# Performance work log

Measured on AMD Instinct MI355X. Metric: run time of the kernel, lower is better.

## Reference

```python
import jax, jax.numpy as jnp
import numpy as np


def _nearest_resize(x, Hl, Wl):
    # x: [B, Hf, Wf] -> [B, Hl, Wl], PyTorch F.interpolate(mode='nearest') semantics:
    # src_idx = floor(out_idx * in_size / out_size)
    B, Hf, Wf = x.shape
    ri = (jnp.arange(Hl) * Hf) // Hl
    ci = (jnp.arange(Wl) * Wf) // Wl
    return x[:, ri[:, None], ci[None, :]]


def _nearest_centroid(f, c):
    # f: [B, C, H, W], c: [K, C]
    # argmin_k ||f - c_k||_2 over channels == argmin of squared distance
    f2 = jnp.sum(f * f, axis=1)                       # [B, H, W]
    c2 = jnp.sum(c * c, axis=1)                       # [K]
    cross = jnp.einsum('bchw,kc->bkhw', f, c)         # [B, K, H, W]
    d2 = f2[:, None] - 2.0 * cross + c2[None, :, None, None]
    return jnp.argmin(d2, axis=1)                     # [B, H, W] int


def setup_inputs() -> dict:
    key = jax.random.key(0)
    k1, k2, k3, k4, k5, k6 = jax.random.split(key, 6)
    B, C, Hf, Wf = 4, 256, 64, 128
    K = 19  # class_num
    Hl, Wl = 512, 1024
    return {
        'feature_s2t': jax.random.normal(k1, (B, C, Hf, Wf), dtype=jnp.float32),
        'feature_target': jax.random.normal(k2, (B, C, Hf, Wf), dtype=jnp.float32),
        'label_s2t': jax.random.randint(k3, (B, Hl, Wl), 0, K, dtype=jnp.int64) if jax.config.jax_enable_x64 else jax.random.randint(k3, (B, Hl, Wl), 0, K, dtype=jnp.int32),
        'label_target': jax.random.randint(k4, (B, Hl, Wl), 0, K, dtype=jnp.int32),
        'centroid_s2t': jax.random.normal(k5, (K, C), dtype=jnp.float32),
        'centroid_target': jax.random.normal(k6, (K, C), dtype=jnp.float32),
    }


def reference(feature_s2t, feature_target, label_s2t, label_target, centroid_s2t, centroid_target):
    # feature_s2t is matched against the TARGET-domain centroids and vice versa
    # (cross assignment, exactly as in the torch forward).
    mask_s2t = _nearest_centroid(feature_s2t, centroid_target)     # [B, Hf, Wf]
    mask_target = _nearest_centroid(feature_target, centroid_s2t)  # [B, Hf, Wf]
    Hl, Wl = label_s2t.shape[1], label_s2t.shape[2]
    mask_s2t = _nearest_resize(mask_s2t, Hl, Wl).astype(jnp.int32)
    Hl2, Wl2 = label_target.shape[1], label_target.shape[2]
    mask_target = _nearest_resize(mask_target, Hl2, Wl2).astype(jnp.int32)
    return (mask_s2t, mask_target)
```

## Files before the change

kernel.cpp:

```cpp
#include <hip/hip_runtime.h>

#define K   19
#define C   256
#define HF  64
#define WF  128
#define HW  (HF * WF)
#define BB  4
#define HL  512
#define WL  1024

#define TAU 0.03f

#define CPAD 264
#define DPAD 66

typedef __attribute__((ext_vector_type(8)))  short bf16x8;
typedef __attribute__((ext_vector_type(16))) float f32x16;

__global__ __launch_bounds__(256, 4) void centroid_mask_kernel(
    const float* __restrict__ feat0,
    const float* __restrict__ feat1,
    const float* __restrict__ cent0,
    const float* __restrict__ cent1,
    int* __restrict__ out)
{
    __shared__ __align__(16) unsigned short chi[K * CPAD];
    __shared__ __align__(16) unsigned short clo[K * CPAD];
    __shared__ float  dbuf[4][16][DPAD];
    __shared__ double c2p[K][8];
    __shared__ double sc2d[K];
    __shared__ float  sc2f[K];

    const int map = blockIdx.y;
    const float* __restrict__ feat = (map == 0) ? feat0 : feat1;
    const float* __restrict__ cent = (map == 0) ? cent0 : cent1;

    const int tid  = threadIdx.x;
    const int lane = tid & 63;
    const int wv   = __builtin_amdgcn_readfirstlane(tid >> 6);

    for (int i = tid; i < K * C; i += 256) {
        const int k = i >> 8, c = i & (C - 1);
        const unsigned u = __float_as_uint(cent[i]);
        const float r = __uint_as_float(u) - __uint_as_float(u & 0xffff0000u);
        chi[k * CPAD + c] = (unsigned short)(u >> 16);
        clo[k * CPAD + c] = (unsigned short)(__float_as_uint(r) >> 16);
    }
    if (tid < K * 8) {
        const int k = tid >> 3, sl = tid & 7;
        const float* cp = cent + k * C + sl * 32;
        double s = 0.0;
        #pragma unroll
        for (int j = 0; j < 32; ++j) { double v = (double)cp[j]; s = fma(v, v, s); }
        c2p[k][sl] = s;
    }
    __syncthreads();
    if (tid < K) {
        double s = 0.0;
        #pragma unroll
        for (int j = 0; j < 8; ++j) s += c2p[tid][j];
        sc2d[tid] = s;
        sc2f[tid] = (float)s;
    }

    const int hl2  = (lane >> 5) & 1;
    const int pp   = blockIdx.x * 128 + wv * 32 + (lane & 31);
    const int hw   = pp & (HW - 1);
    const int b    = pp >> 13;

    const float* __restrict__ fp = feat + (size_t)b * C * HW + hw;
    const int bidx = min(lane & 31, 18) * CPAD + hl2 * 8;

    f32x16 acc;
    #pragma unroll
    for (int r = 0; r < 16; ++r) acc[r] = 0.f;

    #pragma unroll
    for (int s = 0; s < 16; ++s) {
        const int cb = s * 16 + hl2 * 8;
        float fv[8];
        #pragma unroll
        for (int j = 0; j < 8; ++j)
            fv[j] = fp[(size_t)(cb + j) * HW];

        union { unsigned u[4]; bf16x8 v; } ah, al, bh, bl;
        #pragma unroll
        for (int j = 0; j < 4; ++j) {
            const unsigned u0 = __float_as_uint(fv[2*j]);
            const unsigned u1 = __float_as_uint(fv[2*j+1]);
            ah.u[j] = (u0 >> 16) | (u1 & 0xffff0000u);
            const float r0 = fv[2*j]   - __uint_as_float(u0 & 0xffff0000u);
            const float r1 = fv[2*j+1] - __uint_as_float(u1 & 0xffff0000u);
            al.u[j] = (__float_as_uint(r0) >> 16)
                    | (__float_as_uint(r1) & 0xffff0000u);
        }
        bh.v = *(const bf16x8*)&chi[bidx + s * 16];
        bl.v = *(const bf16x8*)&clo[bidx + s * 16];

        acc = __builtin_amdgcn_mfma_f32_32x32x16_bf16(ah.v, bh.v, acc, 0, 0, 0);
        acc = __builtin_amdgcn_mfma_f32_32x32x16_bf16(ah.v, bl.v, acc, 0, 0, 0);
        acc = __builtin_amdgcn_mfma_f32_32x32x16_bf16(al.v, bh.v, acc, 0, 0, 0);
    }

    {
        float* dst = &dbuf[wv][0][hl2 * 32 + (lane & 31)];
        #pragma unroll
        for (int r = 0; r < 16; ++r) dst[r * DPAD] = acc[r];
    }
    __syncthreads();

    if (tid < 128) {
        const int el  = tid & 63;
        const int ep  = tid;
        const int tl  = ep >> 5, px = ep & 31;
        const int h   = (px >> 2) & 1;
        const int reg = (px & 3) | ((px >> 3) << 2);
        const int bse = h * 32;

        const int ppx = blockIdx.x * 128 + ep;
        const int phw = ppx & (HW - 1);
        const int pb  = ppx >> 13;

        float d[K];
        #pragma unroll
        for (int k = 0; k < K; ++k)
            d[k] = sc2f[k] - 2.0f * dbuf[tl][reg][bse + k];

        int best = 0; float m1 = d[0];
        #pragma unroll
        for (int k = 1; k < K; ++k) if (d[k] < m1) { m1 = d[k]; best = k; }

        unsigned cmask = 0u;
        #pragma unroll
        for (int k = 0; k < K; ++k) if (d[k] - m1 < TAU) cmask |= (1u << k);

        const bool need = (cmask & (cmask - 1)) != 0u;
        unsigned long long ball = __ballot(need);
        while (ball) {
            const int sx = (int)__builtin_ctzll(ball);
            ball &= ball - 1;
            const unsigned pm  = __shfl(cmask, sx, 64);
            const int      fhw = __shfl(phw,   sx, 64);
            const int      fb  = __shfl(pb,    sx, 64);
            const float* __restrict__ fcol = feat + (size_t)fb * C * HW + fhw;

            const int c0 = el << 2;
            double pf[4];
            #pragma unroll
            for (int j = 0; j < 4; ++j)
                pf[j] = (double)fcol[(size_t)(c0 + j) * HW];

            double bd = 1e300; int bi = 0;
            unsigned mm = pm;
            while (mm) {
                const int k = (int)__builtin_ctz(mm);
                mm &= mm - 1;
                const float* __restrict__ ck = cent + (size_t)k * C + c0;
                double s = 0.0;
                #pragma unroll
                for (int j = 0; j < 4; ++j)
                    s = fma(pf[j], (double)ck[j], s);
                #pragma unroll
                for (int off = 1; off < 64; off <<= 1)
                    s += __shfl_xor(s, off, 64);
                const double dk = sc2d[k] - 2.0 * s;
                if (dk < bd) { bd = dk; bi = k; }
            }
            if (el == sx) best = bi;
        }

        const int w  = phw & (WF - 1);
        const int hh = phw >> 7;
        int4 v = make_int4(best, best, best, best);
        int* __restrict__ ob = out + (size_t)map * (BB * HL * WL)
                                   + (size_t)pb * (HL * WL)
                                   + (size_t)(hh * 8) * WL + (size_t)(w * 8);
        #pragma unroll
        for (int r = 0; r < 8; ++r) {
            *(int4*)(ob + (size_t)r * WL)     = v;
            *(int4*)(ob + (size_t)r * WL + 4) = v;
        }
    }
}

extern "C" void kernel_launch(void* const* d_in, const int* in_sizes, int n_in,
                              void* d_out, int out_size, void* d_ws, size_t ws_size,
                              hipStream_t stream) {
    const float* feature_s2t     = (const float*)d_in[0];
    const float* feature_target  = (const float*)d_in[1];
    const float* centroid_s2t    = (const float*)d_in[4];
    const float* centroid_target = (const float*)d_in[5];
    int* out = (int*)d_out;

    dim3 grid(32768 / 128, 2);
    dim3 block(256);
    hipLaunchKernelGGL(centroid_mask_kernel, grid, block, 0, stream,
                       feature_s2t, feature_target,
                       centroid_target, centroid_s2t, out);
}
```

Measured before the change: 23.79 us.

## Split channel reduction across four waves per pixel group with float2 loads

Block grows to 512 threads. Each wave now handles 64 pixels, using two accumulators fed by float2 feature loads, over a quarter of the channel dimension. The four partial dot-product tiles go into a shared-memory pool that is reused from the centroid bf16 buffers, and they are summed in the argmin stage. This splits the serial K-loop across waves to shorten per-wave latency and widens global loads, at the cost of an extra barrier, a larger LDS partial buffer and a different fp32 summation order.

```diff
diff --git a/kernel.cpp b/kernel.cpp
--- a/kernel.cpp
+++ b/kernel.cpp
@@ -13,24 +13,29 @@
 
 #define CPAD 264
 #define DPAD 66
+#define CHI_BYTES  (K * CPAD * 2)
+#define DBUF_BYTES (16 * 16 * DPAD * 4)
+#define POOL_BYTES DBUF_BYTES
 
 typedef __attribute__((ext_vector_type(8)))  short bf16x8;
 typedef __attribute__((ext_vector_type(16))) float f32x16;
 
-__global__ __launch_bounds__(256, 4) void centroid_mask_kernel(
+__global__ __launch_bounds__(512, 4) void centroid_mask_kernel(
     const float* __restrict__ feat0,
     const float* __restrict__ feat1,
     const float* __restrict__ cent0,
     const float* __restrict__ cent1,
     int* __restrict__ out)
 {
-    __shared__ __align__(16) unsigned short chi[K * CPAD];
-    __shared__ __align__(16) unsigned short clo[K * CPAD];
-    __shared__ float  dbuf[4][16][DPAD];
+    __shared__ __align__(16) unsigned char pool[POOL_BYTES];
     __shared__ double c2p[K][8];
     __shared__ double sc2d[K];
     __shared__ float  sc2f[K];
 
+    unsigned short* __restrict__ chi = (unsigned short*)pool;
+    unsigned short* __restrict__ clo = (unsigned short*)(pool + CHI_BYTES);
+    float*          __restrict__ dbf = (float*)pool;
+
     const int map = blockIdx.y;
     const float* __restrict__ feat = (map == 0) ? feat0 : feat1;
     const float* __restrict__ cent = (map == 0) ? cent0 : cent1;
@@ -38,8 +43,10 @@
     const int tid  = threadIdx.x;
     const int lane = tid & 63;
     const int wv   = __builtin_amdgcn_readfirstlane(tid >> 6);
-
-    for (int i = tid; i < K * C; i += 256) {
+    const int pxg  = wv >> 2;
+    const int khq  = wv & 3;
+
+    for (int i = tid; i < K * C; i += 512) {
         const int k = i >> 8, c = i & (C - 1);
         const unsigned u = __float_as_uint(cent[i]);
         const float r = __uint_as_float(u) - __uint_as_float(u & 0xffff0000u);
@@ -63,58 +70,84 @@
         sc2f[tid] = (float)s;
     }
 
-    const int hl2  = (lane >> 5) & 1;
-    const int pp   = blockIdx.x * 128 + wv * 32 + (lane & 31);
-    const int hw   = pp & (HW - 1);
-    const int b    = pp >> 13;
-
-    const float* __restrict__ fp = feat + (size_t)b * C * HW + hw;
-    const int bidx = min(lane & 31, 18) * CPAD + hl2 * 8;
-
-    f32x16 acc;
+    const int hl2 = (lane >> 5) & 1;
+    const int pg  = blockIdx.x * 128 + pxg * 64;
+    const int hw0 = pg & (HW - 1);
+    const int b   = pg >> 13;
+
+    const float2* __restrict__ fp2 =
+        (const float2*)(feat + (size_t)b * C * HW + hw0);
+    const int cb0  = khq * 64 + hl2 * 8;
+    const int bidx = min(lane & 31, 18) * CPAD + khq * 64 + hl2 * 8;
+
+    f32x16 acc0, acc1;
     #pragma unroll
-    for (int r = 0; r < 16; ++r) acc[r] = 0.f;
+    for (int r = 0; r < 16; ++r) { acc0[r] = 0.f; acc1[r] = 0.f; }
 
     #pragma unroll
-    for (int s = 0; s < 16; ++s) {
-        const int cb = s * 16 + hl2 * 8;
-        float fv[8];
+    for (int s = 0; s < 4; ++s) {
+        float2 fv[8];
         #pragma unroll
         for (int j = 0; j < 8; ++j)
-            fv[j] = fp[(size_t)(cb + j) * HW];
-
-        union { unsigned u[4]; bf16x8 v; } ah, al, bh, bl;
+            fv[j] = fp2[(size_t)(cb0 + s * 16 + j) * (HW / 2) + (lane & 31)];
+
+        union { unsigned u[4]; bf16x8 v; } ah0, al0, ah1, al1, bh, bl;
         #pragma unroll
         for (int j = 0; j < 4; ++j) {
-            const unsigned u0 = __float_as_uint(fv[2*j]);
-            const unsigned u1 = __float_as_uint(fv[2*j+1]);
-            ah.u[j] = (u0 >> 16) | (u1 & 0xffff0000u);
-            const float r0 = fv[2*j]   - __uint_as_float(u0 & 0xffff0000u);
-            const float r1 = fv[2*j+1] - __uint_as_float(u1 & 0xffff0000u);
-            al.u[j] = (__float_as_uint(r0) >> 16)
-                    | (__float_as_uint(r1) & 0xffff0000u);
+            {
+                const unsigned u0 = __float_as_uint(fv[2*j].x);
+                const unsigned u1 = __float_as_uint(fv[2*j+1].x);
+                ah0.u[j] = (u0 >> 16) | (u1 & 0xffff0000u);
+                const float r0 = fv[2*j].x   - __uint_as_float(u0 & 0xffff0000u);
+                const float r1 = fv[2*j+1].x - __uint_as_float(u1 & 0xffff0000u);
+                al0.u[j] = (__float_as_uint(r0) >> 16)
+                         | (__float_as_uint(r1) & 0xffff0000u);
+            }
+            {
+                const unsigned u0 = __float_as_uint(fv[2*j].y);
+                const unsigned u1 = __float_as_uint(fv[2*j+1].y);
+                ah1.u[j] = (u0 >> 16) | (u1 & 0xffff0000u);
+                const float r0 = fv[2*j].y   - __uint_as_float(u0 & 0xffff0000u);
+                const float r1 = fv[2*j+1].y - __uint_as_float(u1 & 0xffff0000u);
+                al1.u[j] = (__float_as_uint(r0) >> 16)
+                         | (__float_as_uint(r1) & 0xffff0000u);
+            }
         }
         bh.v = *(const bf16x8*)&chi[bidx + s * 16];
         bl.v = *(const bf16x8*)&clo[bidx + s * 16];
 
-        acc = __builtin_amdgcn_mfma_f32_32x32x16_bf16(ah.v, bh.v, acc, 0, 0, 0);
-        acc = __builtin_amdgcn_mfma_f32_32x32x16_bf16(ah.v, bl.v, acc, 0, 0, 0);
-        acc = __builtin_amdgcn_mfma_f32_32x32x16_bf16(al.v, bh.v, acc, 0, 0, 0);
-    }
+        acc0 = __builtin_amdgcn_mfma_f32_32x32x16_bf16(ah0.v, bh.v, acc0, 0, 0, 0);
+        acc0 = __builtin_amdgcn_mfma_f32_32x32x16_bf16(ah0.v, bl.v, acc0, 0, 0, 0);
+        acc0 = __builtin_amdgcn_mfma_f32_32x32x16_bf16(al0.v, bh.v, acc0, 0, 0, 0);
+        acc1 = __builtin_amdgcn_mfma_f32_32x32x16_bf16(ah1.v, bh.v, acc1, 0, 0, 0);
+        acc1 = __builtin_amdgcn_mfma_f32_32x32x16_bf16(ah1.v, bl.v, acc1, 0, 0, 0);
+        acc1 = __builtin_amdgcn_mfma_f32_32x32x16_bf16(al1.v, bh.v, acc1, 0, 0, 0);
+    }
+
+    __syncthreads();
 
     {
-        float* dst = &dbuf[wv][0][hl2 * 32 + (lane & 31)];
-        #pragma unroll
-        for (int r = 0; r < 16; ++r) dst[r * DPAD] = acc[r];
+        const int slot0 = ((pxg * 4 + khq) * 2 + 0) * 16;
+        const int slot1 = ((pxg * 4 + khq) * 2 + 1) * 16;
+        float* d0 = &dbf[slot0 * DPAD + hl2 * 32 + (lane & 31)];
+        float* d1 = &dbf[slot1 * DPAD + hl2 * 32 + (lane & 31)];
+        #pragma unroll
+        for (int r = 0; r < 16; ++r) {
+            d0[r * DPAD] = acc0[r];
+            d1[r * DPAD] = acc1[r];
+        }
     }
     __syncthreads();
 
     if (tid < 128) {
         const int el  = tid & 63;
         const int ep  = tid;
-        const int tl  = ep >> 5, px = ep & 31;
-        const int h   = (px >> 2) & 1;
-        const int reg = (px & 3) | ((px >> 3) << 2);
+        const int epg = ep >> 6;
+        const int px  = ep & 63;
+        const int tl  = px & 1;
+        const int m   = px >> 1;
+        const int h   = (m >> 2) & 1;
+        const int reg = (m & 3) | ((m >> 3) << 2);
         const int bse = h * 32;
 
         const int ppx = blockIdx.x * 128 + ep;
@@ -123,9 +156,14 @@
 
         float d[K];
         #pragma unroll
-        for (int k = 0; k < K; ++k)
-            d[k] = sc2f[k] - 2.0f * dbuf[tl][reg][bse + k];
-
+        for (int k = 0; k < K; ++k) {
+            const float s =
+                (dbf[(((epg*4+0)*2+tl)*16 + reg) * DPAD + bse + k]
+               + dbf[(((epg*4+1)*2+tl)*16 + reg) * DPAD + bse + k])
+              + (dbf[(((epg*4+2)*2+tl)*16 + reg) * DPAD + bse + k]
+               + dbf[(((epg*4+3)*2+tl)*16 + reg) * DPAD + bse + k]);
+            d[k] = sc2f[k] - 2.0f * s;
+        }
         int best = 0; float m1 = d[0];
         #pragma unroll
         for (int k = 1; k < K; ++k) if (d[k] < m1) { m1 = d[k]; best = k; }
@@ -193,7 +231,7 @@
     int* out = (int*)d_out;
 
     dim3 grid(32768 / 128, 2);
-    dim3 block(256);
+    dim3 block(512);
     hipLaunchKernelGGL(centroid_mask_kernel, grid, block, 0, stream,
                        feature_s2t, feature_target,
                        centroid_target, centroid_s2t, out);
```

Measured after the change: 24.25 us. No clear change (+1.9%).
